# Performance work log

Hardware: AMD Instinct MI355X
Metric: run time of the kernel (lower is better)

The kernel has to match this reference:

```python
import jax, jax.numpy as jnp
import numpy as np

BETA = 0.7
NUM_STEPS = 25
HID = 256
SPIKE_DIM = 128
COORD_DIM = 64
IN_DIM = SPIKE_DIM + COORD_DIM  # 192
BATCH = 131072


def setup_inputs() -> dict:
    key = jax.random.key(0)
    ks = jax.random.split(key, 8)
    s = lambda fan_in: 1.0 / np.sqrt(fan_in)
    return {
        "sensor_spikes": jax.random.uniform(ks[0], (BATCH, SPIKE_DIM), dtype=jnp.float32),
        "current_coords": jax.random.normal(ks[1], (BATCH, COORD_DIM), dtype=jnp.float32),
        # nn.Linear weights are [out, in], uniform(-1/sqrt(in), 1/sqrt(in))
        "W0": jax.random.uniform(ks[2], (HID, IN_DIM), jnp.float32, -s(IN_DIM), s(IN_DIM)),
        "b0": jax.random.uniform(ks[3], (HID,), jnp.float32, -s(IN_DIM), s(IN_DIM)),
        "W1": jax.random.uniform(ks[4], (HID, HID), jnp.float32, -s(HID), s(HID)),
        "b1": jax.random.uniform(ks[5], (HID,), jnp.float32, -s(HID), s(HID)),
        "W_out": jax.random.uniform(ks[6], (IN_DIM, HID), jnp.float32, -s(HID), s(HID)),
        "b_out": jax.random.uniform(ks[7], (IN_DIM,), jnp.float32, -s(HID), s(HID)),
    }


def reference(sensor_spikes, current_coords, W0, b0, W1, b1, W_out, b_out):
    x = jnp.concatenate([sensor_spikes, current_coords], axis=-1)  # [B, 192]
    B = x.shape[0]
    # Layer-0 drive is x every timestep (the original re-feeds x each step),
    # so its pre-activation current is step-invariant.
    c0 = x @ W0.T + b0  # [B, HID]

    def lif(v, current):
        v = BETA * v + (1.0 - BETA) * current
        spikes = (v >= 1.0).astype(v.dtype)
        v = v * (1.0 - spikes)
        return v, spikes

    def step(carry, _):
        v0, v1 = carry
        v0, s0 = lif(v0, c0)
        c1 = s0 @ W1.T + b1
        v1, s1 = lif(v1, c1)
        return (v0, v1), s1

    zeros = jnp.zeros((B, HID), dtype=x.dtype)
    (_, _), s1_seq = jax.lax.scan(step, (zeros, zeros), None, length=NUM_STEPS)
    final_spikes = s1_seq[-1]  # [B, HID]

    out = final_spikes @ W_out.T + b_out  # [B, 192]
    next_action = jnp.sign(final_spikes)  # spikes are 0/1 -> sign == spikes
    next_coords = out[:, -COORD_DIM:]
    return next_action, next_coords
```

## Files before the change

kernel.cpp:

```cpp
#include <hip/hip_runtime.h>
#include <stdint.h>

#define BATCH_N   131072
#define HID       256
#define SPIKE_DIM 128
#define COORD_DIM 64
#define IN_DIM    192
#define STEPS     25
#define TILE      64
#define SUBT      4
#define BLOCK     512

typedef float f4  __attribute__((ext_vector_type(4)));
typedef short bf8 __attribute__((ext_vector_type(8)));
typedef unsigned short us4 __attribute__((ext_vector_type(4)));

#define W1T_OFF  24576
#define WOT_OFF  90112
#define SCAL_OFF 106496

static __device__ __forceinline__ unsigned short f2bf(float f) {
  union { float f; unsigned u; } v; v.f = f;
  unsigned r = v.u + 0x7FFF + ((v.u >> 16) & 1);
  return (unsigned short)(r >> 16);
}

__global__ __launch_bounds__(256)
void prep_kernel(const float* __restrict__ W0,
                 const float* __restrict__ W1,
                 const float* __restrict__ Wout,
                 const float* __restrict__ b1,
                 float* __restrict__ ws) {
  const int t = threadIdx.x, b = blockIdx.x;
  if (b == 512) {
    unsigned u = __float_as_uint(fmaxf(b1[t], 0.f));
    #pragma unroll
    for (int o = 1; o < 64; o <<= 1) {
      unsigned v = __shfl_xor(u, o);
      u = v > u ? v : u;
    }
    if ((t & 63) == 0) atomicMax((unsigned*)(ws + SCAL_OFF), u);
    return;
  }
  int idx = b * 256 + t;
  if (idx < HID*IN_DIM) {
    ((unsigned short*)ws)[idx] = f2bf(W0[idx]);
  }
  int i1 = idx - HID*IN_DIM;
  if (i1 >= 0 && i1 < HID*HID) {
    int j = i1 >> 8, i = i1 & 255;
    ws[W1T_OFF + i1] = W1[i*HID + j];
  }
  int i2 = idx - (HID*IN_DIM + HID*HID);
  if (i2 >= 0 && i2 < HID*COORD_DIM) {
    int k = i2 >> 6, c = i2 & 63;
    ws[WOT_OFF + i2] = Wout[(SPIKE_DIM + c)*HID + k];
  }
  if (b < 64) {
    f4 v = ((const f4*)W1)[idx];
    float m = fmaxf(fmaxf(v.x, v.y), fmaxf(v.z, v.w));
    m = fmaxf(m, 0.f);
    unsigned u = __float_as_uint(m);
    #pragma unroll
    for (int o = 1; o < 64; o <<= 1) {
      unsigned w = __shfl_xor(u, o);
      u = w > u ? w : u;
    }
    if ((t & 63) == 0) atomicMax((unsigned*)(ws + SCAL_OFF + 1), u);
  }
}

#define STAGE_LOAD(e0n)                                              \
  {                                                                  \
    const f4* sp4 = (const f4*)(spk + (size_t)(e0n) * SPIKE_DIM);    \
    const f4* cr4 = (const f4*)(crd + (size_t)(e0n) * COORD_DIM);    \
    r0 = __builtin_nontemporal_load(&sp4[tid]);                      \
    r1 = __builtin_nontemporal_load(&sp4[tid + 512]);                \
    r2 = __builtin_nontemporal_load(&sp4[tid + 1024]);               \
    r3 = __builtin_nontemporal_load(&sp4[tid + 1536]);               \
    r4 = __builtin_nontemporal_load(&cr4[tid]);                      \
    r5 = __builtin_nontemporal_load(&cr4[tid + 512]);                \
  }

#define CV(h, r) { h.x = f2bf(r.x); h.y = f2bf(r.y); h.z = f2bf(r.z); h.w = f2bf(r.w); }

#define STAGE_WRITE(dst)                                             \
  {                                                                  \
    const int es = tid >> 5, js = (tid & 31) * 4;                    \
    const int ec = tid >> 4, jc = SPIKE_DIM + (tid & 15) * 4;        \
    us4 h;                                                           \
    CV(h, r0) *(us4*)&(dst)[(es     )*200 + js] = h;                 \
    CV(h, r1) *(us4*)&(dst)[(es + 16)*200 + js] = h;                 \
    CV(h, r2) *(us4*)&(dst)[(es + 32)*200 + js] = h;                 \
    CV(h, r3) *(us4*)&(dst)[(es + 48)*200 + js] = h;                 \
    CV(h, r4) *(us4*)&(dst)[(ec     )*200 + jc] = h;                 \
    CV(h, r5) *(us4*)&(dst)[(ec + 32)*200 + jc] = h;                 \
  }

__global__ __launch_bounds__(BLOCK, 4)
void snn_kernel(const float* __restrict__ spk,
                const float* __restrict__ crd,
                const float* __restrict__ W0,
                const float* __restrict__ b0,
                const float* __restrict__ b1,
                const float* __restrict__ bout,
                const float* __restrict__ ws,
                float* __restrict__ out) {
  __shared__ unsigned short sbuf[2*TILE*200];
  __shared__ unsigned cnt2[2*32];

  const int tid  = threadIdx.x;
  const int lane = tid & 63;
  const int wv   = tid >> 6;
  const int quad = lane >> 4;
  const int l15  = lane & 15;
  const int i4   = lane * 4;
  const int tile0 = blockIdx.x * SUBT;

  if (tid < 64) cnt2[tid] = 0;

  f4 r0, r1, r2, r3, r4, r5;
  STAGE_LOAD(tile0 * TILE)

  const unsigned short* W0b = (const unsigned short*)ws;
  float b0n[2];
  b0n[0] = b0[wv*32 + l15];
  b0n[1] = b0[wv*32 + 16 + l15];
  bf8 bfr[2][6];
  #pragma unroll
  for (int n = 0; n < 2; ++n)
    #pragma unroll
    for (int kc = 0; kc < 6; ++kc)
      bfr[n][kc] = *(const bf8*)&W0b[(size_t)(wv*32 + n*16 + l15)*IN_DIM
                                     + kc*32 + quad*8];
  const float b1mx = ws[SCAL_OFF];
  const float w1pm = ws[SCAL_OFF + 1];
  const float bc = bout[SPIKE_DIM + lane];
  const int eb = wv * 8;

  STAGE_WRITE(sbuf)
  __syncthreads();

  for (int s = 0; s < SUBT; ++s) {
    unsigned short* bufc = &sbuf[(s & 1) * TILE*200];
    unsigned short* bufn = &sbuf[((s + 1) & 1) * TILE*200];
    unsigned* cw = &cnt2[(s & 1) * 32];
    const int e0s = (tile0 + s) * TILE;
    const bool more = (s + 1 < SUBT);

    if (more) STAGE_LOAD((tile0 + s + 1) * TILE)

    #pragma unroll
    for (int mh = 0; mh < 2; ++mh) {
      f4 acc[2][2];
      #pragma unroll
      for (int m = 0; m < 2; ++m)
        #pragma unroll
        for (int n = 0; n < 2; ++n)
          { acc[m][n].x = acc[m][n].y = acc[m][n].z = acc[m][n].w = 0.f; }
      #pragma unroll
      for (int kc = 0; kc < 6; ++kc) {
        #pragma unroll
        for (int m = 0; m < 2; ++m) {
          bf8 a = *(const bf8*)&bufc[((mh*2 + m)*16 + l15)*200 + kc*32 + quad*8];
          acc[m][0] = __builtin_amdgcn_mfma_f32_16x16x32_bf16(a, bfr[0][kc], acc[m][0], 0, 0, 0);
          acc[m][1] = __builtin_amdgcn_mfma_f32_16x16x32_bf16(a, bfr[1][kc], acc[m][1], 0, 0, 0);
        }
      }
      #pragma unroll
      for (int m = 0; m < 2; ++m) {
        unsigned lo = 0, hi = 0;
        #pragma unroll
        for (int n = 0; n < 2; ++n) {
          lo += (acc[m][n].x + b0n[n] >= 0.90f) ? 1u       : 0u;
          lo += (acc[m][n].y + b0n[n] >= 0.90f) ? (1u<<16) : 0u;
          hi += (acc[m][n].z + b0n[n] >= 0.90f) ? 1u       : 0u;
          hi += (acc[m][n].w + b0n[n] >= 0.90f) ? (1u<<16) : 0u;
        }
        lo += __shfl_xor(lo, 1, 16); hi += __shfl_xor(hi, 1, 16);
        lo += __shfl_xor(lo, 2, 16); hi += __shfl_xor(hi, 2, 16);
        lo += __shfl_xor(lo, 4, 16); hi += __shfl_xor(hi, 4, 16);
        lo += __shfl_xor(lo, 8, 16); hi += __shfl_xor(hi, 8, 16);
        if (l15 == 0) {
          atomicAdd(&cw[((mh*2 + m)*4 + quad)*2 + 0], lo);
          atomicAdd(&cw[((mh*2 + m)*4 + quad)*2 + 1], hi);
        }
      }
    }
    __syncthreads();

    unsigned fastm = 0;
    #pragma unroll
    for (int ee = 0; ee < 8; ++ee) {
      const int el = eb + ee;
      unsigned w = cw[(el >> 2)*2 + ((el >> 1) & 1)];
      unsigned nspk = (w >> ((el & 1)*16)) & 0xFFFFu;
      if (b1mx + w1pm * (float)nspk < 0.97f) fastm |= (1u << ee);
    }
    if (lane < 4) cw[wv*4 + lane] = 0;

    #pragma unroll
    for (int ee = 0; ee < 8; ++ee) {
      if (fastm & (1u << ee)) {
        const int e = e0s + eb + ee;
        f4 z; z.x = z.y = z.z = z.w = 0.f;
        __builtin_nontemporal_store(z, (f4*)&out[(size_t)e*HID + i4]);
        __builtin_nontemporal_store(bc,
            &out[(size_t)BATCH_N*HID + (size_t)e*COORD_DIM + lane]);
      }
    }

    if (__builtin_expect(fastm != 0xFFu, 0)) {
      const float* W1T = ws + W1T_OFF;
      const float* WoT = ws + WOT_OFF;
      f4 b0v = *(const f4*)&b0[i4];
      f4 b1v = *(const f4*)&b1[i4];
      for (int ee = 0; ee < 8; ++ee) {
        if (fastm & (1u << ee)) continue;
        const int e = e0s + eb + ee;

        float cx = 0.f, cy = 0.f, cz = 0.f, cw_ = 0.f;
        const float* q0 = W0 + (size_t)(i4+0)*IN_DIM;
        const float* q1 = W0 + (size_t)(i4+1)*IN_DIM;
        const float* q2 = W0 + (size_t)(i4+2)*IN_DIM;
        const float* q3 = W0 + (size_t)(i4+3)*IN_DIM;
        const float* xs_ = spk + (size_t)e*SPIKE_DIM;
        const float* xc_ = crd + (size_t)e*COORD_DIM;
        for (int j = 0; j < SPIKE_DIM; ++j) {
          float xj = xs_[j];
          cx = fmaf(xj, q0[j], cx); cy = fmaf(xj, q1[j], cy);
          cz = fmaf(xj, q2[j], cz); cw_ = fmaf(xj, q3[j], cw_);
        }
        for (int j = 0; j < COORD_DIM; ++j) {
          float xj = xc_[j];
          cx = fmaf(xj, q0[SPIKE_DIM+j], cx); cy = fmaf(xj, q1[SPIKE_DIM+j], cy);
          cz = fmaf(xj, q2[SPIKE_DIM+j], cz); cw_ = fmaf(xj, q3[SPIKE_DIM+j], cw_);
        }
        const float c0x = cx + b0v.x, c0y = cy + b0v.y;
        const float c0z = cz + b0v.z, c0w = cw_ + b0v.w;

        float v0x=0.f, v0y=0.f, v0z=0.f, v0w=0.f;
        float v1x=0.f, v1y=0.f, v1z=0.f, v1w=0.f;
        float s1x=0.f, s1y=0.f, s1z=0.f, s1w=0.f;
        unsigned long long mm;

        for (int t = 0; t < STEPS; ++t) {
          bool sp;
          unsigned long long m0, m1, m2, m3;
          v0x = __fmul_rn(0.7f, v0x) + __fmul_rn(0.3f, c0x);
          sp = (v0x >= 1.0f); m0 = __ballot(sp); if (sp) v0x = 0.f;
          v0y = __fmul_rn(0.7f, v0y) + __fmul_rn(0.3f, c0y);
          sp = (v0y >= 1.0f); m1 = __ballot(sp); if (sp) v0y = 0.f;
          v0z = __fmul_rn(0.7f, v0z) + __fmul_rn(0.3f, c0z);
          sp = (v0z >= 1.0f); m2 = __ballot(sp); if (sp) v0z = 0.f;
          v0w = __fmul_rn(0.7f, v0w) + __fmul_rn(0.3f, c0w);
          sp = (v0w >= 1.0f); m3 = __ballot(sp); if (sp) v0w = 0.f;

          float c1x = b1v.x, c1y = b1v.y, c1z = b1v.z, c1w = b1v.w;
          f4 wcur; wcur.x = wcur.y = wcur.z = wcur.w = 0.f;
          int have = 0;
          #define PROCQ(MASK, Q)                                                  \
            mm = (MASK);                                                          \
            while (mm) {                                                          \
              int l = __builtin_ctzll(mm); mm &= mm - 1;                          \
              f4 wn = *(const f4*)&W1T[(l*4 + (Q))*HID + i4];                     \
              if (have) { c1x += wcur.x; c1y += wcur.y; c1z += wcur.z; c1w += wcur.w; } \
              wcur = wn; have = 1;                                                \
            }
          PROCQ(m0, 0)
          PROCQ(m1, 1)
          PROCQ(m2, 2)
          PROCQ(m3, 3)
          #undef PROCQ
          if (have) { c1x += wcur.x; c1y += wcur.y; c1z += wcur.z; c1w += wcur.w; }

          v1x = __fmul_rn(0.7f, v1x) + __fmul_rn(0.3f, c1x);
          sp = (v1x >= 1.0f); s1x = sp ? 1.f : 0.f; if (sp) v1x = 0.f;
          v1y = __fmul_rn(0.7f, v1y) + __fmul_rn(0.3f, c1y);
          sp = (v1y >= 1.0f); s1y = sp ? 1.f : 0.f; if (sp) v1y = 0.f;
          v1z = __fmul_rn(0.7f, v1z) + __fmul_rn(0.3f, c1z);
          sp = (v1z >= 1.0f); s1z = sp ? 1.f : 0.f; if (sp) v1z = 0.f;
          v1w = __fmul_rn(0.7f, v1w) + __fmul_rn(0.3f, c1w);
          sp = (v1w >= 1.0f); s1w = sp ? 1.f : 0.f; if (sp) v1w = 0.f;
        }

        f4 res; res.x = s1x; res.y = s1y; res.z = s1z; res.w = s1w;
        __builtin_nontemporal_store(res, (f4*)&out[(size_t)e*HID + i4]);

        unsigned long long f0 = __ballot(s1x > 0.5f);
        unsigned long long f1 = __ballot(s1y > 0.5f);
        unsigned long long f2 = __ballot(s1z > 0.5f);
        unsigned long long f3 = __ballot(s1w > 0.5f);
        float cacc = bc;
        #define CPROCQ(MASK, Q)                                 \
          mm = (MASK);                                          \
          while (mm) {                                          \
            int l = __builtin_ctzll(mm); mm &= mm - 1;          \
            cacc += WoT[(l*4 + (Q))*COORD_DIM + lane];          \
          }
        CPROCQ(f0, 0)
        CPROCQ(f1, 1)
        CPROCQ(f2, 2)
        CPROCQ(f3, 3)
        #undef CPROCQ
        __builtin_nontemporal_store(cacc,
            &out[(size_t)BATCH_N*HID + (size_t)e*COORD_DIM + lane]);
      }
    }

    if (more) {
      STAGE_WRITE(bufn)
      __syncthreads();
    }
  }
}

extern "C" void kernel_launch(void* const* d_in, const int* in_sizes, int n_in,
                              void* d_out, int out_size, void* d_ws, size_t ws_size,
                              hipStream_t stream) {
  (void)in_sizes; (void)n_in; (void)out_size; (void)ws_size;
  const float* spk = (const float*)d_in[0];
  const float* crd = (const float*)d_in[1];
  const float* W0  = (const float*)d_in[2];
  const float* b0  = (const float*)d_in[3];
  const float* W1  = (const float*)d_in[4];
  const float* b1  = (const float*)d_in[5];
  const float* Wo  = (const float*)d_in[6];
  const float* bo  = (const float*)d_in[7];
  float* ws  = (float*)d_ws;
  float* out = (float*)d_out;

  hipMemsetAsync(ws + SCAL_OFF, 0, 8, stream);
  hipLaunchKernelGGL(prep_kernel, dim3(513), dim3(256), 0, stream, W0, W1, Wo, b1, ws);
  hipLaunchKernelGGL(snn_kernel, dim3(BATCH_N/(TILE*SUBT)), dim3(BLOCK), 0, stream,
                     spk, crd, W0, b0, b1, bo, ws, out);
}
```

Before: 354.0 us.

## Pre-convert inputs to bf16 fragment layout and drop LDS staging

Adds a prep kernel that converts the spike and coordinate inputs to bf16, stored in workspace in MFMA fragment order. The main kernel then loads A fragments straight from global memory instead of staging through double-buffered shared memory, and each block handles 2 tiles instead of 4. A fallback path converts from fp32 in place when the workspace is too small. This removes the LDS writes, reads and barriers, at the cost of an extra pass that writes and rereads roughly 50MB of bf16 data.

```diff
diff --git a/kernel.cpp b/kernel.cpp
--- a/kernel.cpp
+++ b/kernel.cpp
@@ -8,7 +8,6 @@
 #define IN_DIM    192
 #define STEPS     25
 #define TILE      64
-#define SUBT      4
 #define BLOCK     512
 
 typedef float f4  __attribute__((ext_vector_type(4)));
@@ -18,6 +17,8 @@
 #define W1T_OFF  24576
 #define WOT_OFF  90112
 #define SCAL_OFF 106496
+#define XB16_OFF 106512
+#define XB16_NEED_BYTES ((size_t)XB16_OFF*4 + (size_t)BATCH_N*IN_DIM*2)
 
 static __device__ __forceinline__ unsigned short f2bf(float f) {
   union { float f; unsigned u; } v; v.f = f;
@@ -70,33 +71,53 @@
   }
 }
 
-#define STAGE_LOAD(e0n)                                              \
-  {                                                                  \
-    const f4* sp4 = (const f4*)(spk + (size_t)(e0n) * SPIKE_DIM);    \
-    const f4* cr4 = (const f4*)(crd + (size_t)(e0n) * COORD_DIM);    \
-    r0 = __builtin_nontemporal_load(&sp4[tid]);                      \
-    r1 = __builtin_nontemporal_load(&sp4[tid + 512]);                \
-    r2 = __builtin_nontemporal_load(&sp4[tid + 1024]);               \
-    r3 = __builtin_nontemporal_load(&sp4[tid + 1536]);               \
-    r4 = __builtin_nontemporal_load(&cr4[tid]);                      \
-    r5 = __builtin_nontemporal_load(&cr4[tid + 512]);                \
-  }
-
-#define CV(h, r) { h.x = f2bf(r.x); h.y = f2bf(r.y); h.z = f2bf(r.z); h.w = f2bf(r.w); }
-
-#define STAGE_WRITE(dst)                                             \
-  {                                                                  \
-    const int es = tid >> 5, js = (tid & 31) * 4;                    \
-    const int ec = tid >> 4, jc = SPIKE_DIM + (tid & 15) * 4;        \
-    us4 h;                                                           \
-    CV(h, r0) *(us4*)&(dst)[(es     )*200 + js] = h;                 \
-    CV(h, r1) *(us4*)&(dst)[(es + 16)*200 + js] = h;                 \
-    CV(h, r2) *(us4*)&(dst)[(es + 32)*200 + js] = h;                 \
-    CV(h, r3) *(us4*)&(dst)[(es + 48)*200 + js] = h;                 \
-    CV(h, r4) *(us4*)&(dst)[(ec     )*200 + jc] = h;                 \
-    CV(h, r5) *(us4*)&(dst)[(ec + 32)*200 + jc] = h;                 \
-  }
-
+__global__ __launch_bounds__(256)
+void prep_x(const float* __restrict__ spk,
+            const float* __restrict__ crd,
+            float* __restrict__ ws) {
+  const int tid  = threadIdx.x;
+  const int w    = blockIdx.x * 4 + (tid >> 6);
+  const int lane = tid & 63;
+  const int l15  = lane & 15;
+  const int quad = lane >> 4;
+  const int c    = w / 6, kc = w - c * 6;
+  const float* src = (kc < 4)
+      ? spk + (size_t)(c*16 + l15)*SPIKE_DIM + kc*32 + quad*8
+      : crd + (size_t)(c*16 + l15)*COORD_DIM + (kc-4)*32 + quad*8;
+  f4 a = *(const f4*)src;
+  f4 b = *((const f4*)src + 1);
+  uint4 o;
+  o.x = (unsigned)f2bf(a.x) | ((unsigned)f2bf(a.y) << 16);
+  o.y = (unsigned)f2bf(a.z) | ((unsigned)f2bf(a.w) << 16);
+  o.z = (unsigned)f2bf(b.x) | ((unsigned)f2bf(b.y) << 16);
+  o.w = (unsigned)f2bf(b.z) | ((unsigned)f2bf(b.w) << 16);
+  unsigned short* xb16 = (unsigned short*)(ws + XB16_OFF);
+  *(uint4*)&xb16[((size_t)w*64 + lane)*8] = o;
+}
+
+#define LOAD_A1(dst, gm_)                                                    \
+  { const size_t fb_ = ((size_t)(gm_)*6)*64 + lane;                          \
+    _Pragma("unroll")                                                        \
+    for (int kc_ = 0; kc_ < 6; ++kc_)                                        \
+      dst[kc_] = *(const bf8*)&xb16[(fb_ + (size_t)kc_*64)*8]; }
+
+#define LOAD_A0(dst, gm_)                                                    \
+  { const int er_ = (gm_)*16 + l15;                                          \
+    _Pragma("unroll")                                                        \
+    for (int kc_ = 0; kc_ < 6; ++kc_) {                                      \
+      const float* sA_ = (kc_ < 4)                                           \
+        ? spk + (size_t)er_*SPIKE_DIM + kc_*32 + quad*8                      \
+        : crd + (size_t)er_*COORD_DIM + (kc_-4)*32 + quad*8;                 \
+      f4 x0_ = *(const f4*)sA_;                                              \
+      f4 x1_ = *((const f4*)sA_ + 1);                                        \
+      bf8 t_;                                                                \
+      t_[0]=(short)f2bf(x0_.x); t_[1]=(short)f2bf(x0_.y);                    \
+      t_[2]=(short)f2bf(x0_.z); t_[3]=(short)f2bf(x0_.w);                    \
+      t_[4]=(short)f2bf(x1_.x); t_[5]=(short)f2bf(x1_.y);                    \
+      t_[6]=(short)f2bf(x1_.z); t_[7]=(short)f2bf(x1_.w);                    \
+      dst[kc_] = t_; } }
+
+template<int TILED>
 __global__ __launch_bounds__(BLOCK, 4)
 void snn_kernel(const float* __restrict__ spk,
                 const float* __restrict__ crd,
@@ -106,7 +127,6 @@
                 const float* __restrict__ bout,
                 const float* __restrict__ ws,
                 float* __restrict__ out) {
-  __shared__ unsigned short sbuf[2*TILE*200];
   __shared__ unsigned cnt2[2*32];
 
   const int tid  = threadIdx.x;
@@ -115,14 +135,12 @@
   const int quad = lane >> 4;
   const int l15  = lane & 15;
   const int i4   = lane * 4;
-  const int tile0 = blockIdx.x * SUBT;
+  const int tileBase = blockIdx.x * 2;
 
   if (tid < 64) cnt2[tid] = 0;
 
-  f4 r0, r1, r2, r3, r4, r5;
-  STAGE_LOAD(tile0 * TILE)
-
-  const unsigned short* W0b = (const unsigned short*)ws;
+  const unsigned short* W0b  = (const unsigned short*)ws;
+  const unsigned short* xb16 = (const unsigned short*)(ws + XB16_OFF);
   float b0n[2];
   b0n[0] = b0[wv*32 + l15];
   b0n[1] = b0[wv*32 + 16 + l15];
@@ -138,53 +156,41 @@
   const float bc = bout[SPIKE_DIM + lane];
   const int eb = wv * 8;
 
-  STAGE_WRITE(sbuf)
   __syncthreads();
-
-  for (int s = 0; s < SUBT; ++s) {
-    unsigned short* bufc = &sbuf[(s & 1) * TILE*200];
-    unsigned short* bufn = &sbuf[((s + 1) & 1) * TILE*200];
-    unsigned* cw = &cnt2[(s & 1) * 32];
-    const int e0s = (tile0 + s) * TILE;
-    const bool more = (s + 1 < SUBT);
-
-    if (more) STAGE_LOAD((tile0 + s + 1) * TILE)
-
-    #pragma unroll
-    for (int mh = 0; mh < 2; ++mh) {
-      f4 acc[2][2];
-      #pragma unroll
-      for (int m = 0; m < 2; ++m)
-        #pragma unroll
-        for (int n = 0; n < 2; ++n)
-          { acc[m][n].x = acc[m][n].y = acc[m][n].z = acc[m][n].w = 0.f; }
+  #pragma unroll
+  for (int s = 0; s < 2; ++s) {
+    unsigned* cw = &cnt2[s * 32];
+    const int e0s = (tileBase + s) * TILE;
+
+    #pragma unroll
+    for (int m = 0; m < 4; ++m) {
+      const int gm = (tileBase + s)*4 + m;
+      bf8 afr[6];
+      if (TILED) { LOAD_A1(afr, gm) } else { LOAD_A0(afr, gm) }
+      f4 ac0, ac1;
+      ac0.x = ac0.y = ac0.z = ac0.w = 0.f;
+      ac1.x = ac1.y = ac1.z = ac1.w = 0.f;
       #pragma unroll
       for (int kc = 0; kc < 6; ++kc) {
-        #pragma unroll
-        for (int m = 0; m < 2; ++m) {
-          bf8 a = *(const bf8*)&bufc[((mh*2 + m)*16 + l15)*200 + kc*32 + quad*8];
-          acc[m][0] = __builtin_amdgcn_mfma_f32_16x16x32_bf16(a, bfr[0][kc], acc[m][0], 0, 0, 0);
-          acc[m][1] = __builtin_amdgcn_mfma_f32_16x16x32_bf16(a, bfr[1][kc], acc[m][1], 0, 0, 0);
-        }
+        ac0 = __builtin_amdgcn_mfma_f32_16x16x32_bf16(afr[kc], bfr[0][kc], ac0, 0, 0, 0);
+        ac1 = __builtin_amdgcn_mfma_f32_16x16x32_bf16(afr[kc], bfr[1][kc], ac1, 0, 0, 0);
       }
-      #pragma unroll
-      for (int m = 0; m < 2; ++m) {
-        unsigned lo = 0, hi = 0;
-        #pragma unroll
-        for (int n = 0; n < 2; ++n) {
-          lo += (acc[m][n].x + b0n[n] >= 0.90f) ? 1u       : 0u;
-          lo += (acc[m][n].y + b0n[n] >= 0.90f) ? (1u<<16) : 0u;
-          hi += (acc[m][n].z + b0n[n] >= 0.90f) ? 1u       : 0u;
-          hi += (acc[m][n].w + b0n[n] >= 0.90f) ? (1u<<16) : 0u;
-        }
-        lo += __shfl_xor(lo, 1, 16); hi += __shfl_xor(hi, 1, 16);
-        lo += __shfl_xor(lo, 2, 16); hi += __shfl_xor(hi, 2, 16);
-        lo += __shfl_xor(lo, 4, 16); hi += __shfl_xor(hi, 4, 16);
-        lo += __shfl_xor(lo, 8, 16); hi += __shfl_xor(hi, 8, 16);
-        if (l15 == 0) {
-          atomicAdd(&cw[((mh*2 + m)*4 + quad)*2 + 0], lo);
-          atomicAdd(&cw[((mh*2 + m)*4 + quad)*2 + 1], hi);
-        }
+      unsigned lo = 0, hi = 0;
+      lo += (ac0.x + b0n[0] >= 0.90f) ? 1u       : 0u;
+      lo += (ac1.x + b0n[1] >= 0.90f) ? 1u       : 0u;
+      lo += (ac0.y + b0n[0] >= 0.90f) ? 0x10000u : 0u;
+      lo += (ac1.y + b0n[1] >= 0.90f) ? 0x10000u : 0u;
+      hi += (ac0.z + b0n[0] >= 0.90f) ? 1u       : 0u;
+      hi += (ac1.z + b0n[1] >= 0.90f) ? 1u       : 0u;
+      hi += (ac0.w + b0n[0] >= 0.90f) ? 0x10000u : 0u;
+      hi += (ac1.w + b0n[1] >= 0.90f) ? 0x10000u : 0u;
+      lo += __shfl_xor(lo, 1, 16); hi += __shfl_xor(hi, 1, 16);
+      lo += __shfl_xor(lo, 2, 16); hi += __shfl_xor(hi, 2, 16);
+      lo += __shfl_xor(lo, 4, 16); hi += __shfl_xor(hi, 4, 16);
+      lo += __shfl_xor(lo, 8, 16); hi += __shfl_xor(hi, 8, 16);
+      if (l15 == 0) {
+        atomicAdd(&cw[(m*4 + quad)*2 + 0], lo);
+        atomicAdd(&cw[(m*4 + quad)*2 + 1], hi);
       }
     }
     __syncthreads();
@@ -197,7 +203,6 @@
       unsigned nspk = (w >> ((el & 1)*16)) & 0xFFFFu;
       if (b1mx + w1pm * (float)nspk < 0.97f) fastm |= (1u << ee);
     }
-    if (lane < 4) cw[wv*4 + lane] = 0;
 
     #pragma unroll
     for (int ee = 0; ee < 8; ++ee) {
@@ -307,18 +312,13 @@
             &out[(size_t)BATCH_N*HID + (size_t)e*COORD_DIM + lane]);
       }
     }
-
-    if (more) {
-      STAGE_WRITE(bufn)
-      __syncthreads();
-    }
   }
 }
 
 extern "C" void kernel_launch(void* const* d_in, const int* in_sizes, int n_in,
                               void* d_out, int out_size, void* d_ws, size_t ws_size,
                               hipStream_t stream) {
-  (void)in_sizes; (void)n_in; (void)out_size; (void)ws_size;
+  (void)in_sizes; (void)n_in; (void)out_size;
   const float* spk = (const float*)d_in[0];
   const float* crd = (const float*)d_in[1];
   const float* W0  = (const float*)d_in[2];
@@ -332,6 +332,13 @@
 
   hipMemsetAsync(ws + SCAL_OFF, 0, 8, stream);
   hipLaunchKernelGGL(prep_kernel, dim3(513), dim3(256), 0, stream, W0, W1, Wo, b1, ws);
-  hipLaunchKernelGGL(snn_kernel, dim3(BATCH_N/(TILE*SUBT)), dim3(BLOCK), 0, stream,
-                     spk, crd, W0, b0, b1, bo, ws, out);
-}
+  if (ws_size >= XB16_NEED_BYTES) {
+    hipLaunchKernelGGL(prep_x, dim3(BATCH_N/16*6/4), dim3(256), 0, stream,
+                       spk, crd, ws);
+    hipLaunchKernelGGL((snn_kernel<1>), dim3(BATCH_N/(TILE*2)), dim3(BLOCK), 0,
+                       stream, spk, crd, W0, b0, b1, bo, ws, out);
+  } else {
+    hipLaunchKernelGGL((snn_kernel<0>), dim3(BATCH_N/(TILE*2)), dim3(BLOCK), 0,
+                       stream, spk, crd, W0, b0, b1, bo, ws, out);
+  }
+}
```

New measurement: 343.0 us. 1.03x faster.
